# Kernel optimization log

Hardware: AMD Instinct MI355X
Metric: run time of the kernel (lower is better)

## Reference

```python
import jax, jax.numpy as jnp
import numpy as np

NB_HEAD = 8
SIZE_PER_HEAD = 64
EMB = 512  # word embedding dim; output_dim = NB_HEAD*SIZE_PER_HEAD = 512
B, S = 8, 4096


def setup_inputs() -> dict:
    key = jax.random.key(0)
    ks = jax.random.split(key, 8)
    return {
        "Q_seq": jax.random.normal(ks[0], (B, S, EMB), dtype=jnp.float32),
        "K_seq": jax.random.normal(ks[1], (B, S, EMB), dtype=jnp.float32),
        "V_seq": jax.random.normal(ks[2], (B, S, EMB), dtype=jnp.float32),
        "Q_len": jax.random.randint(ks[3], (B, 1), 0, S, dtype=jnp.int32),
        "V_len": jax.random.randint(ks[4], (B, 1), 0, SIZE_PER_HEAD, dtype=jnp.int32),
        "WQ": jax.random.normal(ks[5], (EMB, NB_HEAD * SIZE_PER_HEAD), dtype=jnp.float32),
        "WK": jax.random.normal(ks[6], (EMB, NB_HEAD * SIZE_PER_HEAD), dtype=jnp.float32),
        "WV": jax.random.normal(ks[7], (EMB, NB_HEAD * SIZE_PER_HEAD), dtype=jnp.float32),
    }


def _proj_heads(x, W):
    # [B,S,E] @ [E,H*d] -> [B,H,S,d]
    y = jnp.einsum('bse,eo->bso', x, W)
    y = y.reshape(y.shape[0], y.shape[1], NB_HEAD, SIZE_PER_HEAD)
    return jnp.transpose(y, (0, 2, 1, 3))


def reference(Q_seq, K_seq, V_seq, Q_len, V_len, WQ, WK, WV):
    H, d = NB_HEAD, SIZE_PER_HEAD
    Q = _proj_heads(Q_seq, WQ)  # [B,H,S,d]
    K = _proj_heads(K_seq, WK)
    V = _proj_heads(V_seq, WV)

    A = (Q * K) / jnp.asarray(d, Q.dtype) ** 0.5  # elementwise, [B,H,S,d]

    # TF code transposes A to [B,d,S,H] and masks along axis 1 (size d) using
    # V_len, then transposes back. Equivalent: additive mask on the LAST axis.
    vmask = jax.nn.one_hot(V_len[:, 0], d, dtype=A.dtype)       # [B,d]
    vmask = 1.0 - jnp.cumsum(vmask, axis=1)                      # [B,d]
    A = A - (1.0 - vmask)[:, None, None, :] * 1e12

    A = jax.nn.softmax(A, axis=-1)  # softmax over d (last axis), as tf.nn.softmax

    O = A * V                              # [B,H,S,d]
    O = jnp.transpose(O, (0, 2, 1, 3))     # [B,S,H,d]
    O = O.reshape(O.shape[0], O.shape[1], H * d)  # [B,S,H*d]

    # multiplicative mask over sequence axis using Q_len
    qmask = jax.nn.one_hot(Q_len[:, 0], O.shape[1], dtype=O.dtype)  # [B,S]
    qmask = 1.0 - jnp.cumsum(qmask, axis=1)
    return O * qmask[:, :, None]
```

## Files before the change

kernel.cpp:

```cpp
#include <hip/hip_runtime.h>

typedef unsigned short u16;
typedef _Float16 f16;
typedef _Float16 f16x4 __attribute__((ext_vector_type(4)));
typedef _Float16 f16x8 __attribute__((ext_vector_type(8)));
typedef float    f32x4 __attribute__((ext_vector_type(4)));

#define BATCH 8
#define SEQ   4096
#define EMB   512
#define NCOL  512

__global__ __launch_bounds__(256) void prep_w(
    const float* __restrict__ Wq, const float* __restrict__ Wk,
    const float* __restrict__ Wv, u16* __restrict__ out)
{
  __shared__ u16 tile[64][65];
  const int z = blockIdx.z;
  const float* in = (z < 2) ? Wq : (z < 4) ? Wk : Wv;
  const bool lo = (z == 1 || z == 3);
  u16* o = out + (size_t)z * EMB * NCOL;
  const int r0 = blockIdx.y * 64, c0 = blockIdx.x * 64;
  const int tx = threadIdx.x, ty = threadIdx.y;
#pragma unroll
  for (int i = 0; i < 16; ++i) {
    const int r = ty * 16 + i;
    const float x = in[(size_t)(r0 + r) * NCOL + (c0 + tx)];
    const f16 h = (f16)x;
    const f16 v = lo ? (f16)((x - (float)h) * 16.0f) : h;
    tile[r][tx] = __builtin_bit_cast(u16, v);
  }
  __syncthreads();
#pragma unroll
  for (int i = 0; i < 16; ++i) {
    const int rr = ty * 16 + i;
    o[(size_t)(c0 + rr) * EMB + (r0 + tx)] = tile[tx][rr];
  }
}

#define PLANE 2048
#define BUFSZ (5*PLANE)

__global__ __launch_bounds__(512, 2) void fused_attn(
    const float* __restrict__ Xq, const float* __restrict__ Xk,
    const float* __restrict__ Xv,
    const int* __restrict__ Qlen, const int* __restrict__ Vlen,
    const u16* __restrict__ Wt,
    float* __restrict__ out)
{
  const int b  = blockIdx.z;
  const int s0 = blockIdx.x * 64;
  const int c0 = blockIdx.y * 256;
  const int qlen = Qlen[b];
  const int t = threadIdx.x;

  if (s0 >= qlen) {
    const f32x4 z4 = {0.f, 0.f, 0.f, 0.f};
#pragma unroll
    for (int it = 0; it < 8; ++it) {
      const int f4  = it * 512 + t;
      const int row = f4 >> 6;
      const int col = (f4 & 63) * 4;
      *(f32x4*)(out + (size_t)(b * SEQ + s0 + row) * NCOL + c0 + col) = z4;
    }
    return;
  }
  const int vlen = Vlen[b];
  const int vl = (vlen == 0) ? 64 : vlen;

  __shared__ f16 smem[2 * BUFSZ] __attribute__((aligned(16)));

  const int w    = t >> 6;
  const int lane = t & 63;
  const int quad = lane >> 4;
  const int l15  = lane & 15;

  const int    srow = t >> 3;
  const int    sj   = t & 7;
  const size_t xg   = (size_t)(b * SEQ + s0 + srow) * EMB + sj * 4;
  const int    swo  = srow * 32 + (((sj >> 1) ^ ((srow >> 1) & 3)) * 8) + (sj & 1) * 4;

  const size_t wb = (size_t)(c0 + w * 32 + l15) * EMB + quad * 8;
  const u16* Wqh_g = Wt                + wb;
  const u16* Wql_g = Wt + 1 * EMB*NCOL + wb;
  const u16* Wkh_g = Wt + 2 * EMB*NCOL + wb;
  const u16* Wkl_g = Wt + 3 * EMB*NCOL + wb;
  const u16* Wv_g  = Wt + 4 * EMB*NCOL + wb;

  const int swz = (l15 >> 1) & 3;
  const int ao  = l15 * 32 + ((quad ^ swz) * 8);

  f32x4 accQ[4][2], accK[4][2], accV[4][2];
#pragma unroll
  for (int rt = 0; rt < 4; ++rt)
#pragma unroll
    for (int ct = 0; ct < 2; ++ct) {
      const f32x4 z = {0.f, 0.f, 0.f, 0.f};
      accQ[rt][ct] = z; accK[rt][ct] = z; accV[rt][ct] = z;
    }

  f32x4 rq, rk, rv;

#define LOADX(TT) do { \
    rq = *(const f32x4*)(Xq + xg + (TT) * 32); \
    rk = *(const f32x4*)(Xk + xg + (TT) * 32); \
    rv = *(const f32x4*)(Xv + xg + (TT) * 32); \
  } while (0)

#define STAGE(BOFS) do { \
    f16* p_ = smem + (BOFS); \
    f16x4 qh_, ql_, kh_, kl_, vh_; \
    _Pragma("unroll") \
    for (int j = 0; j < 4; ++j) { \
      const float xq_ = rq[j]; const f16 qhh_ = (f16)xq_; \
      qh_[j] = qhh_; ql_[j] = (f16)((xq_ - (float)qhh_) * 16.0f); \
      const float xk_ = rk[j]; const f16 khh_ = (f16)xk_; \
      kh_[j] = khh_; kl_[j] = (f16)((xk_ - (float)khh_) * 16.0f); \
      vh_[j] = (f16)rv[j]; \
    } \
    *(f16x4*)(p_ + 0 * PLANE + swo) = qh_; \
    *(f16x4*)(p_ + 1 * PLANE + swo) = ql_; \
    *(f16x4*)(p_ + 2 * PLANE + swo) = kh_; \
    *(f16x4*)(p_ + 3 * PLANE + swo) = kl_; \
    *(f16x4*)(p_ + 4 * PLANE + swo) = vh_; \
  } while (0)

#define COMPUTE(BOFS, KK) do { \
    const f16* p_ = smem + (BOFS); \
    const int kk_ = (KK); \
     \
    f16x8 bqh_[2], bql_[2], bkh_[2], bkl_[2], bv_[2]; \
    _Pragma("unroll") \
    for (int ct = 0; ct < 2; ++ct) { \
      const size_t wo_ = (size_t)ct * 16 * EMB + kk_; \
      bqh_[ct] = *(const f16x8*)(Wqh_g + wo_); \
      bql_[ct] = *(const f16x8*)(Wql_g + wo_); \
      bkh_[ct] = *(const f16x8*)(Wkh_g + wo_); \
      bkl_[ct] = *(const f16x8*)(Wkl_g + wo_); \
      bv_ [ct] = *(const f16x8*)(Wv_g  + wo_); \
    } \
     \
    { \
      f16x8 b4_[2]; \
      _Pragma("unroll") \
      for (int ct = 0; ct < 2; ++ct) \
        _Pragma("unroll") \
        for (int jj = 0; jj < 8; ++jj) b4_[ct][jj] = bqh_[ct][jj] * (f16)0.0625f; \
      _Pragma("unroll") \
      for (int rt = 0; rt < 4; ++rt) { \
        const int ao_ = ao + rt * 512; \
        const f16x8 ah_ = *(const f16x8*)(p_ + 0 * PLANE + ao_); \
        const f16x8 al_ = *(const f16x8*)(p_ + 1 * PLANE + ao_); \
        f16x8 a4_; \
        _Pragma("unroll") \
        for (int jj = 0; jj < 8; ++jj) a4_[jj] = ah_[jj] * (f16)0.0625f; \
        _Pragma("unroll") \
        for (int ct = 0; ct < 2; ++ct) { \
          accQ[rt][ct] = __builtin_amdgcn_mfma_f32_16x16x32_f16(ah_, bqh_[ct], accQ[rt][ct], 0, 0, 0); \
          accQ[rt][ct] = __builtin_amdgcn_mfma_f32_16x16x32_f16(a4_, bql_[ct], accQ[rt][ct], 0, 0, 0); \
          accQ[rt][ct] = __builtin_amdgcn_mfma_f32_16x16x32_f16(al_, b4_[ct],  accQ[rt][ct], 0, 0, 0); \
        } \
      } \
    } \
     \
    { \
      f16x8 b4_[2]; \
      _Pragma("unroll") \
      for (int ct = 0; ct < 2; ++ct) \
        _Pragma("unroll") \
        for (int jj = 0; jj < 8; ++jj) b4_[ct][jj] = bkh_[ct][jj] * (f16)0.0625f; \
      _Pragma("unroll") \
      for (int rt = 0; rt < 4; ++rt) { \
        const int ao_ = ao + rt * 512; \
        const f16x8 ah_ = *(const f16x8*)(p_ + 2 * PLANE + ao_); \
        const f16x8 al_ = *(const f16x8*)(p_ + 3 * PLANE + ao_); \
        f16x8 a4_; \
        _Pragma("unroll") \
        for (int jj = 0; jj < 8; ++jj) a4_[jj] = ah_[jj] * (f16)0.0625f; \
        _Pragma("unroll") \
        for (int ct = 0; ct < 2; ++ct) { \
          accK[rt][ct] = __builtin_amdgcn_mfma_f32_16x16x32_f16(ah_, bkh_[ct], accK[rt][ct], 0, 0, 0); \
          accK[rt][ct] = __builtin_amdgcn_mfma_f32_16x16x32_f16(a4_, bkl_[ct], accK[rt][ct], 0, 0, 0); \
          accK[rt][ct] = __builtin_amdgcn_mfma_f32_16x16x32_f16(al_, b4_[ct],  accK[rt][ct], 0, 0, 0); \
        } \
      } \
    } \
     \
    _Pragma("unroll") \
    for (int rt = 0; rt < 4; ++rt) { \
      const int ao_ = ao + rt * 512; \
      const f16x8 av_ = *(const f16x8*)(p_ + 4 * PLANE + ao_); \
      _Pragma("unroll") \
      for (int ct = 0; ct < 2; ++ct) \
        accV[rt][ct] = __builtin_amdgcn_mfma_f32_16x16x32_f16(av_, bv_[ct], accV[rt][ct], 0, 0, 0); \
    } \
  } while (0)

  LOADX(0);
  STAGE(0);
  __syncthreads();

#pragma unroll 1
  for (int tt = 0; tt < 16; tt += 2) {
    LOADX(tt + 1);
    COMPUTE(0, tt * 32);
    STAGE(BUFSZ);
    __syncthreads();
    if (tt < 14) LOADX(tt + 2);
    COMPUTE(BUFSZ, (tt + 1) * 32);
    if (tt < 14) STAGE(0);
    __syncthreads();
  }

#undef LOADX
#undef STAGE
#undef COMPUTE

  const float scale = 0.125f;
  float* smf = (float*)smem;

  float eA[4][2][4];
  float lm[4][4], lsum[4][4];

#pragma unroll
  for (int rt = 0; rt < 4; ++rt) {
#pragma unroll
    for (int r = 0; r < 4; ++r) {
      float a[2]; bool msk[2];
      float mx = -3.0e38f;
#pragma unroll
      for (int ct = 0; ct < 2; ++ct) {
        const float q = accQ[rt][ct][r];
        const float k = accK[rt][ct][r];
        a[ct] = q * k * scale;
        msk[ct] = ((w & 1) * 32 + ct * 16 + l15) < vl;
        if (msk[ct]) mx = fmaxf(mx, a[ct]);
      }
#pragma unroll
      for (int off = 1; off < 16; off <<= 1) mx = fmaxf(mx, __shfl_xor(mx, off));
      float sum = 0.f;
#pragma unroll
      for (int ct = 0; ct < 2; ++ct) {
        const float e = msk[ct] ? __expf(a[ct] - mx) : 0.0f;
        eA[rt][ct][r] = e;
        sum += e;
      }
#pragma unroll
      for (int off = 1; off < 16; off <<= 1) sum += __shfl_xor(sum, off);
      lm[rt][r] = mx; lsum[rt][r] = sum;
      const int row = rt * 16 + quad * 4 + r;
      if (l15 == 0) {
        smf[(w * 64 + row) * 2 + 0] = mx;
        smf[(w * 64 + row) * 2 + 1] = sum;
      }
    }
  }
  __syncthreads();

#pragma unroll
  for (int rt = 0; rt < 4; ++rt) {
#pragma unroll
    for (int r = 0; r < 4; ++r) {
      const int row = rt * 16 + quad * 4 + r;
      const int s   = s0 + row;
      const float pm = smf[((w ^ 1) * 64 + row) * 2 + 0];
      const float ps = smf[((w ^ 1) * 64 + row) * 2 + 1];
      const float m  = lm[rt][r];
      const float M  = fmaxf(m, pm);
      const float S  = lsum[rt][r] * __expf(m - M) + ps * __expf(pm - M);
      const float qm = (s < qlen) ? 1.0f : 0.0f;
      const float f  = __expf(m - M) * qm / S;
      const size_t ob = (size_t)(b * SEQ + s) * NCOL + c0 + w * 32 + l15;
      out[ob]      = eA[rt][0][r] * f * accV[rt][0][r];
      out[ob + 16] = eA[rt][1][r] * f * accV[rt][1][r];
    }
  }
}

extern "C" void kernel_launch(void* const* d_in, const int* in_sizes, int n_in,
                              void* d_out, int out_size, void* d_ws, size_t ws_size,
                              hipStream_t stream) {
  const float* Xq   = (const float*)d_in[0];
  const float* Xk   = (const float*)d_in[1];
  const float* Xv   = (const float*)d_in[2];
  const int*   Qlen = (const int*)d_in[3];
  const int*   Vlen = (const int*)d_in[4];
  const float* Wq   = (const float*)d_in[5];
  const float* Wk   = (const float*)d_in[6];
  const float* Wv   = (const float*)d_in[7];
  u16*   Wt  = (u16*)d_ws;
  float* out = (float*)d_out;

  dim3 pg(8, 8, 5), pb(64, 4, 1);
  prep_w<<<pg, pb, 0, stream>>>(Wq, Wk, Wv, Wt);

  dim3 g(SEQ / 64, NCOL / 256, BATCH), blk(512, 1, 1);
  fused_attn<<<g, blk, 0, stream>>>(Xq, Xk, Xv, Qlen, Vlen, Wt, out);
}
```

Before: 357.4 us.

## Halve column tile per block to cut registers and raise occupancy

Each block now covers 128 output columns instead of 256, so every wave owns a single 16-column MFMA tile and keeps a third as many accumulators. The softmax over each 64-wide head is now merged across four waves through shared memory instead of two. Launch bounds ask for 4 blocks per SM to exploit the lower register use. The cost is that each block re-stages and re-converts the same X tile, so X is read from global memory twice as often in total, and per-wave MFMA work between syncs shrinks.

```diff
diff --git a/kernel.cpp b/kernel.cpp
--- a/kernel.cpp
+++ b/kernel.cpp
@@ -41,7 +41,7 @@
 #define PLANE 2048
 #define BUFSZ (5*PLANE)
 
-__global__ __launch_bounds__(512, 2) void fused_attn(
+__global__ __launch_bounds__(512, 4) void fused_attn(
     const float* __restrict__ Xq, const float* __restrict__ Xk,
     const float* __restrict__ Xv,
     const int* __restrict__ Qlen, const int* __restrict__ Vlen,
@@ -50,17 +50,17 @@
 {
   const int b  = blockIdx.z;
   const int s0 = blockIdx.x * 64;
-  const int c0 = blockIdx.y * 256;
+  const int c0 = blockIdx.y * 128;
   const int qlen = Qlen[b];
   const int t = threadIdx.x;
 
   if (s0 >= qlen) {
     const f32x4 z4 = {0.f, 0.f, 0.f, 0.f};
 #pragma unroll
-    for (int it = 0; it < 8; ++it) {
+    for (int it = 0; it < 4; ++it) {
       const int f4  = it * 512 + t;
-      const int row = f4 >> 6;
-      const int col = (f4 & 63) * 4;
+      const int row = f4 >> 5;
+      const int col = (f4 & 31) * 4;
       *(f32x4*)(out + (size_t)(b * SEQ + s0 + row) * NCOL + c0 + col) = z4;
     }
     return;
@@ -80,7 +80,7 @@
   const size_t xg   = (size_t)(b * SEQ + s0 + srow) * EMB + sj * 4;
   const int    swo  = srow * 32 + (((sj >> 1) ^ ((srow >> 1) & 3)) * 8) + (sj & 1) * 4;
 
-  const size_t wb = (size_t)(c0 + w * 32 + l15) * EMB + quad * 8;
+  const size_t wb = (size_t)(c0 + w * 16 + l15) * EMB + quad * 8;
   const u16* Wqh_g = Wt                + wb;
   const u16* Wql_g = Wt + 1 * EMB*NCOL + wb;
   const u16* Wkh_g = Wt + 2 * EMB*NCOL + wb;
@@ -90,14 +90,12 @@
   const int swz = (l15 >> 1) & 3;
   const int ao  = l15 * 32 + ((quad ^ swz) * 8);
 
-  f32x4 accQ[4][2], accK[4][2], accV[4][2];
-#pragma unroll
-  for (int rt = 0; rt < 4; ++rt)
-#pragma unroll
-    for (int ct = 0; ct < 2; ++ct) {
-      const f32x4 z = {0.f, 0.f, 0.f, 0.f};
-      accQ[rt][ct] = z; accK[rt][ct] = z; accV[rt][ct] = z;
-    }
+  f32x4 accQ[4], accK[4], accV[4];
+#pragma unroll
+  for (int rt = 0; rt < 4; ++rt) {
+    const f32x4 z = {0.f, 0.f, 0.f, 0.f};
+    accQ[rt] = z; accK[rt] = z; accV[rt] = z;
+  }
 
   f32x4 rq, rk, rv;
 
@@ -129,23 +127,12 @@
     const f16* p_ = smem + (BOFS); \
     const int kk_ = (KK); \
      \
-    f16x8 bqh_[2], bql_[2], bkh_[2], bkl_[2], bv_[2]; \
-    _Pragma("unroll") \
-    for (int ct = 0; ct < 2; ++ct) { \
-      const size_t wo_ = (size_t)ct * 16 * EMB + kk_; \
-      bqh_[ct] = *(const f16x8*)(Wqh_g + wo_); \
-      bql_[ct] = *(const f16x8*)(Wql_g + wo_); \
-      bkh_[ct] = *(const f16x8*)(Wkh_g + wo_); \
-      bkl_[ct] = *(const f16x8*)(Wkl_g + wo_); \
-      bv_ [ct] = *(const f16x8*)(Wv_g  + wo_); \
-    } \
-     \
     { \
-      f16x8 b4_[2]; \
-      _Pragma("unroll") \
-      for (int ct = 0; ct < 2; ++ct) \
-        _Pragma("unroll") \
-        for (int jj = 0; jj < 8; ++jj) b4_[ct][jj] = bqh_[ct][jj] * (f16)0.0625f; \
+      const f16x8 bh_ = *(const f16x8*)(Wqh_g + kk_); \
+      const f16x8 bl_ = *(const f16x8*)(Wql_g + kk_); \
+      f16x8 b4_; \
+      _Pragma("unroll") \
+      for (int jj = 0; jj < 8; ++jj) b4_[jj] = bh_[jj] * (f16)0.0625f; \
       _Pragma("unroll") \
       for (int rt = 0; rt < 4; ++rt) { \
         const int ao_ = ao + rt * 512; \
@@ -154,21 +141,18 @@
         f16x8 a4_; \
         _Pragma("unroll") \
         for (int jj = 0; jj < 8; ++jj) a4_[jj] = ah_[jj] * (f16)0.0625f; \
-        _Pragma("unroll") \
-        for (int ct = 0; ct < 2; ++ct) { \
-          accQ[rt][ct] = __builtin_amdgcn_mfma_f32_16x16x32_f16(ah_, bqh_[ct], accQ[rt][ct], 0, 0, 0); \
-          accQ[rt][ct] = __builtin_amdgcn_mfma_f32_16x16x32_f16(a4_, bql_[ct], accQ[rt][ct], 0, 0, 0); \
-          accQ[rt][ct] = __builtin_amdgcn_mfma_f32_16x16x32_f16(al_, b4_[ct],  accQ[rt][ct], 0, 0, 0); \
-        } \
+        accQ[rt] = __builtin_amdgcn_mfma_f32_16x16x32_f16(ah_, bh_, accQ[rt], 0, 0, 0); \
+        accQ[rt] = __builtin_amdgcn_mfma_f32_16x16x32_f16(a4_, bl_, accQ[rt], 0, 0, 0); \
+        accQ[rt] = __builtin_amdgcn_mfma_f32_16x16x32_f16(al_, b4_, accQ[rt], 0, 0, 0); \
       } \
     } \
      \
     { \
-      f16x8 b4_[2]; \
-      _Pragma("unroll") \
-      for (int ct = 0; ct < 2; ++ct) \
-        _Pragma("unroll") \
-        for (int jj = 0; jj < 8; ++jj) b4_[ct][jj] = bkh_[ct][jj] * (f16)0.0625f; \
+      const f16x8 bh_ = *(const f16x8*)(Wkh_g + kk_); \
+      const f16x8 bl_ = *(const f16x8*)(Wkl_g + kk_); \
+      f16x8 b4_; \
+      _Pragma("unroll") \
+      for (int jj = 0; jj < 8; ++jj) b4_[jj] = bh_[jj] * (f16)0.0625f; \
       _Pragma("unroll") \
       for (int rt = 0; rt < 4; ++rt) { \
         const int ao_ = ao + rt * 512; \
@@ -177,22 +161,19 @@
         f16x8 a4_; \
         _Pragma("unroll") \
         for (int jj = 0; jj < 8; ++jj) a4_[jj] = ah_[jj] * (f16)0.0625f; \
-        _Pragma("unroll") \
-        for (int ct = 0; ct < 2; ++ct) { \
-          accK[rt][ct] = __builtin_amdgcn_mfma_f32_16x16x32_f16(ah_, bkh_[ct], accK[rt][ct], 0, 0, 0); \
-          accK[rt][ct] = __builtin_amdgcn_mfma_f32_16x16x32_f16(a4_, bkl_[ct], accK[rt][ct], 0, 0, 0); \
-          accK[rt][ct] = __builtin_amdgcn_mfma_f32_16x16x32_f16(al_, b4_[ct],  accK[rt][ct], 0, 0, 0); \
-        } \
+        accK[rt] = __builtin_amdgcn_mfma_f32_16x16x32_f16(ah_, bh_, accK[rt], 0, 0, 0); \
+        accK[rt] = __builtin_amdgcn_mfma_f32_16x16x32_f16(a4_, bl_, accK[rt], 0, 0, 0); \
+        accK[rt] = __builtin_amdgcn_mfma_f32_16x16x32_f16(al_, b4_, accK[rt], 0, 0, 0); \
       } \
     } \
      \
-    _Pragma("unroll") \
-    for (int rt = 0; rt < 4; ++rt) { \
-      const int ao_ = ao + rt * 512; \
-      const f16x8 av_ = *(const f16x8*)(p_ + 4 * PLANE + ao_); \
-      _Pragma("unroll") \
-      for (int ct = 0; ct < 2; ++ct) \
-        accV[rt][ct] = __builtin_amdgcn_mfma_f32_16x16x32_f16(av_, bv_[ct], accV[rt][ct], 0, 0, 0); \
+    { \
+      const f16x8 bv_ = *(const f16x8*)(Wv_g + kk_); \
+      _Pragma("unroll") \
+      for (int rt = 0; rt < 4; ++rt) { \
+        const f16x8 av_ = *(const f16x8*)(p_ + 4 * PLANE + ao + rt * 512); \
+        accV[rt] = __builtin_amdgcn_mfma_f32_16x16x32_f16(av_, bv_, accV[rt], 0, 0, 0); \
+      } \
     } \
   } while (0)
 
@@ -219,35 +200,22 @@
   const float scale = 0.125f;
   float* smf = (float*)smem;
 
-  float eA[4][2][4];
-  float lm[4][4], lsum[4][4];
+  float eA[4][4];
 
 #pragma unroll
   for (int rt = 0; rt < 4; ++rt) {
 #pragma unroll
     for (int r = 0; r < 4; ++r) {
-      float a[2]; bool msk[2];
-      float mx = -3.0e38f;
-#pragma unroll
-      for (int ct = 0; ct < 2; ++ct) {
-        const float q = accQ[rt][ct][r];
-        const float k = accK[rt][ct][r];
-        a[ct] = q * k * scale;
-        msk[ct] = ((w & 1) * 32 + ct * 16 + l15) < vl;
-        if (msk[ct]) mx = fmaxf(mx, a[ct]);
-      }
+      const float a = accQ[rt][r] * accK[rt][r] * scale;
+      const bool msk = ((w & 3) * 16 + l15) < vl;
+      float mx = msk ? a : -3.0e38f;
 #pragma unroll
       for (int off = 1; off < 16; off <<= 1) mx = fmaxf(mx, __shfl_xor(mx, off));
-      float sum = 0.f;
-#pragma unroll
-      for (int ct = 0; ct < 2; ++ct) {
-        const float e = msk[ct] ? __expf(a[ct] - mx) : 0.0f;
-        eA[rt][ct][r] = e;
-        sum += e;
-      }
+      const float e = msk ? __expf(a - mx) : 0.0f;
+      eA[rt][r] = e;
+      float sum = e;
 #pragma unroll
       for (int off = 1; off < 16; off <<= 1) sum += __shfl_xor(sum, off);
-      lm[rt][r] = mx; lsum[rt][r] = sum;
       const int row = rt * 16 + quad * 4 + r;
       if (l15 == 0) {
         smf[(w * 64 + row) * 2 + 0] = mx;
@@ -257,22 +225,28 @@
   }
   __syncthreads();
 
+  const int wbase = w & 4;
 #pragma unroll
   for (int rt = 0; rt < 4; ++rt) {
 #pragma unroll
     for (int r = 0; r < 4; ++r) {
       const int row = rt * 16 + quad * 4 + r;
       const int s   = s0 + row;
-      const float pm = smf[((w ^ 1) * 64 + row) * 2 + 0];
-      const float ps = smf[((w ^ 1) * 64 + row) * 2 + 1];
-      const float m  = lm[rt][r];
-      const float M  = fmaxf(m, pm);
-      const float S  = lsum[rt][r] * __expf(m - M) + ps * __expf(pm - M);
+      float pm[4], ps[4];
+      float M = -3.0e38f;
+#pragma unroll
+      for (int j = 0; j < 4; ++j) {
+        pm[j] = smf[((wbase + j) * 64 + row) * 2 + 0];
+        ps[j] = smf[((wbase + j) * 64 + row) * 2 + 1];
+        M = fmaxf(M, pm[j]);
+      }
+      float S = 0.f;
+#pragma unroll
+      for (int j = 0; j < 4; ++j) S += ps[j] * __expf(pm[j] - M);
       const float qm = (s < qlen) ? 1.0f : 0.0f;
-      const float f  = __expf(m - M) * qm / S;
-      const size_t ob = (size_t)(b * SEQ + s) * NCOL + c0 + w * 32 + l15;
-      out[ob]      = eA[rt][0][r] * f * accV[rt][0][r];
-      out[ob + 16] = eA[rt][1][r] * f * accV[rt][1][r];
+      const float f  = __expf(pm[w & 3] - M) * qm / S;
+      const size_t ob = (size_t)(b * SEQ + s) * NCOL + c0 + w * 16 + l15;
+      out[ob] = eA[rt][r] * f * accV[rt][r];
     }
   }
 }
@@ -294,6 +268,6 @@
   dim3 pg(8, 8, 5), pb(64, 4, 1);
   prep_w<<<pg, pb, 0, stream>>>(Wq, Wk, Wv, Wt);
 
-  dim3 g(SEQ / 64, NCOL / 256, BATCH), blk(512, 1, 1);
+  dim3 g(SEQ / 64, NCOL / 128, BATCH), blk(512, 1, 1);
   fused_attn<<<g, blk, 0, stream>>>(Xq, Xk, Xv, Qlen, Vlen, Wt, out);
 }
```

After: 372.5 us. 1.04x slower.
